# Kernel tuning notes

Measured on AMD Instinct MI355X. Metric: run time of the kernel, lower is better.

## Reference

```python
import jax, jax.numpy as jnp
import numpy as np

EMB = 1024
CTX = 32
F_IN, R, F_OUT = 1024, 16, 1024
N_EXP = 16
H1 = 2048   # expert / gating hidden
H2 = 512    # expert output width
B = 8


def _init(key, shape, fan_in):
    return jax.random.normal(key, shape, dtype=jnp.float32) / np.sqrt(fan_in)


def setup_inputs() -> dict:
    key = jax.random.key(0)
    ks = jax.random.split(key, 14)
    return {
        "s": jax.random.normal(ks[0], (B, EMB), dtype=jnp.float32),
        # gating: Linear(EMB,2048) -> ReLU -> Linear(2048,N_EXP) -> Softmax
        "Wg1": _init(ks[1], (EMB, H1), EMB),
        "bg1": jnp.zeros((H1,), jnp.float32),
        "Wg2": _init(ks[2], (H1, N_EXP), H1),
        "bg2": jnp.zeros((N_EXP,), jnp.float32),
        # experts (stacked): Linear(EMB+CTX,2048) -> ReLU -> Linear(2048,512)
        "W1": _init(ks[3], (N_EXP, EMB + CTX, H1), EMB + CTX),
        "b1": jnp.zeros((N_EXP, H1), jnp.float32),
        "W2": _init(ks[4], (N_EXP, H1, H2), H1),
        "b2": jnp.zeros((N_EXP, H2), jnp.float32),
        # decoders
        "WA": _init(ks[5], (H2, F_IN * R), H2),
        "bA": jnp.zeros((F_IN * R,), jnp.float32),
        "WB": _init(ks[6], (H2, R * F_OUT), H2),
        "bB": jnp.zeros((R * F_OUT,), jnp.float32),
    }


def reference(s, Wg1, bg1, Wg2, bg2, W1, b1, W2, b2, WA, bA, WB, bB):
    # gating weights over experts: [B, E]
    weights = jax.nn.softmax(jax.nn.relu(s @ Wg1 + bg1) @ Wg2 + bg2, axis=-1)

    # Expert layer-1. Input is concat([s, one_hot(c)]); since the context part
    # is a one-hot, its contribution is just a row of the context block of W1.
    W1s = W1[:, :EMB, :]              # [E, EMB, H1]
    W1c = W1[:, EMB:, :]              # [E, CTX, H1]
    base = jnp.einsum('bi,eih->ebh', s, W1s) + b1[:, None, :]   # [E, B, H1]
    # h[c,e,b,:] = relu(base[e,b,:] + W1c[e,c,:])
    h = jax.nn.relu(base[None] + jnp.transpose(W1c, (1, 0, 2))[:, :, None, :])  # [C,E,B,H1]

    # Expert layer-2: [C, E, B, H2]
    eo = jnp.einsum('cebh,ehd->cebd', h, W2) + b2[None, :, None, :]

    # softmax-weighted mixture over experts: [C, B, H2]
    z = jnp.einsum('be,cebd->cbd', weights, eo)

    A = (z @ WA + bA).reshape(CTX, B, F_IN, R)
    Bm = (z @ WB + bB).reshape(CTX, B, R, F_OUT)
    return A, Bm
```

## Files before the change

kernel.cpp:

```cpp
#include <hip/hip_runtime.h>
#include <hip/hip_bf16.h>

#define EMB 1024
#define CTX 32
#define NEXP 16
#define H1 2048
#define H2 512
#define NBIG 16384

typedef __attribute__((ext_vector_type(8))) short short8;
typedef __attribute__((ext_vector_type(4))) float floatx4;
typedef const __attribute__((address_space(1))) void* gas_t;
typedef __attribute__((address_space(3))) void* las_t;

__device__ __forceinline__ void gl16(const unsigned short* g, unsigned short* l) {
  __builtin_amdgcn_global_load_lds((gas_t)(const void*)g, (las_t)(void*)l, 16, 0, 0);
}

__device__ inline unsigned short bf_bits(float x) {
  unsigned u = __builtin_bit_cast(unsigned, x);
  u += 0x7fffu + ((u >> 16) & 1u);
  return (unsigned short)(u >> 16);
}
__device__ inline unsigned pk_bf16(float a, float b) {
  return (unsigned)bf_bits(a) | ((unsigned)bf_bits(b) << 16);
}

__global__ void __launch_bounds__(256) k_gate1(const float* __restrict__ s,
                                               const float* __restrict__ Wg1,
                                               const float* __restrict__ bg1,
                                               float* __restrict__ g1) {
  __shared__ float red[16][16][8];
  int t = threadIdx.x;
  int c = t & 15, kk = t >> 4;
  int h = blockIdx.x * 16 + c;
  float acc[8];
#pragma unroll
  for (int b = 0; b < 8; ++b) acc[b] = 0.f;
  int k0 = kk * 64;
  for (int k = k0; k < k0 + 64; ++k) {
    float w = Wg1[(size_t)k * H1 + h];
#pragma unroll
    for (int b = 0; b < 8; ++b) acc[b] += s[b * EMB + k] * w;
  }
#pragma unroll
  for (int b = 0; b < 8; ++b) red[kk][c][b] = acc[b];
  __syncthreads();
  if (t < 128) {
    int cc = t >> 3, b = t & 7;
    float v = 0.f;
#pragma unroll
    for (int q = 0; q < 16; ++q) v += red[q][cc][b];
    int hh = blockIdx.x * 16 + cc;
    v += bg1[hh];
    g1[b * H1 + hh] = fmaxf(v, 0.f);
  }
}

__global__ void __launch_bounds__(256) k_gate2(const float* __restrict__ g1,
                                               const float* __restrict__ Wg2,
                                               const float* __restrict__ bg2,
                                               float* __restrict__ logits) {
  __shared__ float red[256][8];
  int e = blockIdx.x, t = threadIdx.x;
  int k0 = t * 8;
  float wv[8];
#pragma unroll
  for (int j = 0; j < 8; ++j) wv[j] = Wg2[(size_t)(k0 + j) * NEXP + e];
  float acc[8];
#pragma unroll
  for (int b = 0; b < 8; ++b) {
    float4 ga = *(const float4*)&g1[b * H1 + k0];
    float4 gb = *(const float4*)&g1[b * H1 + k0 + 4];
    acc[b] = ga.x * wv[0] + ga.y * wv[1] + ga.z * wv[2] + ga.w * wv[3] +
             gb.x * wv[4] + gb.y * wv[5] + gb.z * wv[6] + gb.w * wv[7];
  }
#pragma unroll
  for (int b = 0; b < 8; ++b) red[t][b] = acc[b];
  __syncthreads();
  for (int off = 128; off > 0; off >>= 1) {
    if (t < off) {
#pragma unroll
      for (int b = 0; b < 8; ++b) red[t][b] += red[t + off][b];
    }
    __syncthreads();
  }
  if (t < 8) logits[t * NEXP + e] = red[0][t] + bg2[e];
}

__global__ void __launch_bounds__(512) k_base(const float* __restrict__ s,
                                              const float* __restrict__ W1,
                                              const float* __restrict__ b1,
                                              float* __restrict__ base) {
  __shared__ float sl[8 * EMB];
  __shared__ float red[8][64][17];
  int t = threadIdx.x;
  int ht = blockIdx.x;
  int e = blockIdx.y;
#pragma unroll
  for (int i = 0; i < 4; ++i) {
    int idx = (t + i * 512) * 4;
    *(float4*)&sl[idx] = *(const float4*)&s[idx];
  }
  __syncthreads();
  int hp = t & 63;
  int kk = t >> 6;
  int h = ht * 128 + hp * 2;
  const float* wp = W1 + (size_t)e * 1056 * H1 + h;
  float a0[8], a1[8];
#pragma unroll
  for (int b = 0; b < 8; ++b) { a0[b] = 0.f; a1[b] = 0.f; }
  int k0 = kk * 128;
  for (int k = k0; k < k0 + 128; ++k) {
    float2 w = *(const float2*)(wp + (size_t)k * H1);
#pragma unroll
    for (int b = 0; b < 8; ++b) {
      float sv = sl[b * EMB + k];
      a0[b] += sv * w.x;
      a1[b] += sv * w.y;
    }
  }
#pragma unroll
  for (int b = 0; b < 8; ++b) {
    red[kk][hp][b * 2] = a0[b];
    red[kk][hp][b * 2 + 1] = a1[b];
  }
  __syncthreads();
  if (t < 64) {
    int hh = ht * 128 + t * 2;
#pragma unroll
    for (int b = 0; b < 8; ++b) {
      float v0 = 0.f, v1 = 0.f;
#pragma unroll
      for (int q = 0; q < 8; ++q) {
        v0 += red[q][t][b * 2];
        v1 += red[q][t][b * 2 + 1];
      }
      float2 bv = *(const float2*)&b1[e * H1 + hh];
      float2 o;
      o.x = v0 + bv.x;
      o.y = v1 + bv.y;
      *(float2*)&base[(size_t)(e * 8 + b) * H1 + hh] = o;
    }
  }
}

__global__ void __launch_bounds__(256) k_packW(const float* __restrict__ src,
                                               unsigned short* __restrict__ dst,
                                               int Nsrc, int Ndst, int n_off,
                                               long sbs, long dbs) {
  __shared__ float tl[64][65];
  int nt = blockIdx.x, kb = blockIdx.y, bz = blockIdx.z, t = threadIdx.x;
  const float* S = src + (size_t)bz * sbs + (size_t)kb * 64 * Nsrc + nt * 64;
  int r = t >> 4, c4 = (t & 15) * 4;
#pragma unroll
  for (int i = 0; i < 4; ++i) {
    int row = r + i * 16;
    float4 v = *(const float4*)&S[(size_t)row * Nsrc + c4];
    *(float4*)&tl[row][c4] = v;
  }
  __syncthreads();
  int nl = t >> 2;
  int cb = (t & 3) * 2;
  int key = nl & 7;
  unsigned short* D = dst + (size_t)bz * dbs +
                      ((size_t)kb * Ndst + n_off + nt * 64 + nl) * 64;
#pragma unroll
  for (int j = 0; j < 2; ++j) {
    int cp = cb + j;
    int k0 = (cp ^ key) * 8;
    union { short8 v; unsigned u[4]; } p;
#pragma unroll
    for (int q = 0; q < 4; ++q)
      p.u[q] = pk_bf16(tl[k0 + 2 * q][nl], tl[k0 + 2 * q + 1][nl]);
    *(short8*)&D[cp * 8] = p.v;
  }
}

__global__ void __launch_bounds__(256) k_h(const float* __restrict__ base,
                                           const float* __restrict__ W1,
                                           unsigned short* __restrict__ h_t) {
  int c = blockIdx.x, e = blockIdx.y;
  int t = threadIdx.x;
  int b = t >> 5, l = t & 31;
  int m = c * 8 + b;
  const float* bp = base + ((size_t)e * 8 + b) * H1;
  const float* cp = W1 + ((size_t)e * 1056 + EMB + c) * H1;
  unsigned short* hp = h_t + (size_t)e * 32 * 256 * 64;
#pragma unroll
  for (int kc = 0; kc < 8; ++kc) {
    int k = kc * 256 + l * 8;
    int kb = k >> 6;
    int cc = (k >> 3) & 7;
    int cpx = cc ^ (b & 7);
    float4 x0 = *(const float4*)&bp[k];
    float4 x1 = *(const float4*)&bp[k + 4];
    float4 y0 = *(const float4*)&cp[k];
    float4 y1 = *(const float4*)&cp[k + 4];
    union { short8 v; unsigned u[4]; } p;
    p.u[0] = pk_bf16(fmaxf(x0.x + y0.x, 0.f), fmaxf(x0.y + y0.y, 0.f));
    p.u[1] = pk_bf16(fmaxf(x0.z + y0.z, 0.f), fmaxf(x0.w + y0.w, 0.f));
    p.u[2] = pk_bf16(fmaxf(x1.x + y1.x, 0.f), fmaxf(x1.y + y1.y, 0.f));
    p.u[3] = pk_bf16(fmaxf(x1.z + y1.z, 0.f), fmaxf(x1.w + y1.w, 0.f));
    *(short8*)&hp[((size_t)kb * 256 + m) * 64 + cpx * 8] = p.v;
  }
}

__global__ void __launch_bounds__(256) k_egemm(const unsigned short* __restrict__ h_t,
                                               const unsigned short* __restrict__ W2t,
                                               float* __restrict__ eo2) {
  __shared__ __align__(16) unsigned short As[4096];
  __shared__ __align__(16) unsigned short Bs[8192];
  int id = blockIdx.x;
  int e = (id & 7) + 8 * ((id >> 3) & 1);
  int r = id >> 4;
  int mt = r & 3, nt = (r >> 2) & 3, ks = (r >> 4) & 1;
  int t = threadIdx.x, lane = t & 63, w = t >> 6;
  int fr = lane & 15, quad = lane >> 4;
  int key = fr & 7;

  const unsigned short* hA = h_t + (size_t)e * 524288 + mt * 4096;
  const unsigned short* wB = W2t + (size_t)e * 1048576 + nt * 8192;

  floatx4 zero4 = {0.f, 0.f, 0.f, 0.f};
  floatx4 acc[4][2];
#pragma unroll
  for (int i = 0; i < 4; ++i) { acc[i][0] = zero4; acc[i][1] = zero4; }

  for (int i = 0; i < 16; ++i) {
    int kb = ks * 16 + i;
    __syncthreads();
    const unsigned short* asrc = hA + (size_t)kb * 16384 + t * 8;
    const unsigned short* bsrc = wB + (size_t)kb * 32768 + t * 8;
    gl16(asrc, &As[t * 8]);
    gl16(asrc + 2048, &As[t * 8 + 2048]);
    gl16(bsrc, &Bs[t * 8]);
    gl16(bsrc + 2048, &Bs[t * 8 + 2048]);
    gl16(bsrc + 4096, &Bs[t * 8 + 4096]);
    gl16(bsrc + 6144, &Bs[t * 8 + 6144]);
    __syncthreads();
#pragma unroll
    for (int ks2 = 0; ks2 < 2; ++ks2) {
      int cof = ((ks2 * 4 + quad) ^ key) * 8;
      short8 bf0 = *(const short8*)&Bs[w * 2048 + fr * 64 + cof];
      short8 bf1 = *(const short8*)&Bs[w * 2048 + 1024 + fr * 64 + cof];
#pragma unroll
      for (int rt = 0; rt < 4; ++rt) {
        short8 af = *(const short8*)&As[rt * 1024 + fr * 64 + cof];
        acc[rt][0] = __builtin_amdgcn_mfma_f32_16x16x32_bf16(af, bf0, acc[rt][0], 0, 0, 0);
        acc[rt][1] = __builtin_amdgcn_mfma_f32_16x16x32_bf16(af, bf1, acc[rt][1], 0, 0, 0);
      }
    }
  }
  float* op = eo2 + (size_t)ks * 2097152;
  int d0 = nt * 128 + w * 32 + fr;
#pragma unroll
  for (int nt2 = 0; nt2 < 2; ++nt2) {
    int d = d0 + nt2 * 16;
#pragma unroll
    for (int rt = 0; rt < 4; ++rt) {
#pragma unroll
      for (int i = 0; i < 4; ++i) {
        int gm = mt * 64 + rt * 16 + quad * 4 + i;
        op[(((size_t)(gm >> 3) * NEXP + e) * 8 + (gm & 7)) * H2 + d] = acc[rt][nt2][i];
      }
    }
  }
}

__global__ void __launch_bounds__(256) k_mix(const float* __restrict__ eo2,
                                             const float* __restrict__ logits,
                                             const float* __restrict__ b2,
                                             unsigned short* __restrict__ z_t) {
  int c = blockIdx.x, half = blockIdx.y, t = threadIdx.x;
  int b = t >> 5;
  int dc = half * 32 + (t & 31);
  int d0 = dc * 8;
  int m = c * 8 + b;
  float lg[16];
  float mx = -1e30f;
#pragma unroll
  for (int e = 0; e < 16; ++e) {
    lg[e] = logits[b * NEXP + e];
    mx = fmaxf(mx, lg[e]);
  }
  float sum = 0.f;
#pragma unroll
  for (int e = 0; e < 16; ++e) {
    lg[e] = __expf(lg[e] - mx);
    sum += lg[e];
  }
  float inv = 1.f / sum;
  float o[8];
#pragma unroll
  for (int j = 0; j < 8; ++j) o[j] = 0.f;
#pragma unroll
  for (int e = 0; e < 16; ++e) {
    float wl = lg[e] * inv;
    const float* p = &eo2[(((size_t)c * NEXP + e) * 8 + b) * H2 + d0];
    float4 x0 = *(const float4*)p;
    float4 x1 = *(const float4*)(p + 4);
    float4 y0 = *(const float4*)(p + 2097152);
    float4 y1 = *(const float4*)(p + 2097152 + 4);
    float4 v0 = *(const float4*)&b2[e * H2 + d0];
    float4 v1 = *(const float4*)&b2[e * H2 + d0 + 4];
    o[0] += wl * (x0.x + y0.x + v0.x);
    o[1] += wl * (x0.y + y0.y + v0.y);
    o[2] += wl * (x0.z + y0.z + v0.z);
    o[3] += wl * (x0.w + y0.w + v0.w);
    o[4] += wl * (x1.x + y1.x + v1.x);
    o[5] += wl * (x1.y + y1.y + v1.y);
    o[6] += wl * (x1.z + y1.z + v1.z);
    o[7] += wl * (x1.w + y1.w + v1.w);
  }
  union { short8 v; unsigned u[4]; } p;
#pragma unroll
  for (int q = 0; q < 4; ++q) p.u[q] = pk_bf16(o[2 * q], o[2 * q + 1]);
  int kb = dc >> 3;
  int cpx = (dc & 7) ^ (b & 7);
  *(short8*)&z_t[((size_t)kb * 256 + m) * 64 + cpx * 8] = p.v;
}

__global__ void __launch_bounds__(256) k_lora(const unsigned short* __restrict__ z_t,
                                              const unsigned short* __restrict__ Wab_t,
                                              const float* __restrict__ bA,
                                              const float* __restrict__ bB,
                                              float* __restrict__ out) {
  __shared__ __align__(16) unsigned short As[8192];
  __shared__ __align__(16) unsigned short Bs[8192];
  int id = blockIdx.x;
  int nt = id & 255, mt = id >> 8;
  int t = threadIdx.x, lane = t & 63, w = t >> 6;
  int fr = lane & 15, quad = lane >> 4;
  int key = fr & 7;

  const unsigned short* zA = z_t + mt * 8192;
  const unsigned short* wB = Wab_t + (size_t)nt * 8192;

  floatx4 zero4 = {0.f, 0.f, 0.f, 0.f};
  floatx4 acc[8][2];
#pragma unroll
  for (int i = 0; i < 8; ++i) { acc[i][0] = zero4; acc[i][1] = zero4; }

  for (int kb = 0; kb < 8; ++kb) {
    __syncthreads();
    const unsigned short* asrc = zA + (size_t)kb * 16384 + t * 8;
    const unsigned short* bsrc = wB + (size_t)kb * 2097152 + t * 8;
    gl16(asrc, &As[t * 8]);
    gl16(asrc + 2048, &As[t * 8 + 2048]);
    gl16(asrc + 4096, &As[t * 8 + 4096]);
    gl16(asrc + 6144, &As[t * 8 + 6144]);
    gl16(bsrc, &Bs[t * 8]);
    gl16(bsrc + 2048, &Bs[t * 8 + 2048]);
    gl16(bsrc + 4096, &Bs[t * 8 + 4096]);
    gl16(bsrc + 6144, &Bs[t * 8 + 6144]);
    __syncthreads();
#pragma unroll
    for (int ks2 = 0; ks2 < 2; ++ks2) {
      int cof = ((ks2 * 4 + quad) ^ key) * 8;
      short8 bf0 = *(const short8*)&Bs[w * 2048 + fr * 64 + cof];
      short8 bf1 = *(const short8*)&Bs[w * 2048 + 1024 + fr * 64 + cof];
#pragma unroll
      for (int rt = 0; rt < 8; ++rt) {
        short8 af = *(const short8*)&As[rt * 1024 + fr * 64 + cof];
        acc[rt][0] = __builtin_amdgcn_mfma_f32_16x16x32_bf16(af, bf0, acc[rt][0], 0, 0, 0);
        acc[rt][1] = __builtin_amdgcn_mfma_f32_16x16x32_bf16(af, bf1, acc[rt][1], 0, 0, 0);
      }
    }
  }
  int nb0 = nt * 128 + w * 32 + fr;
#pragma unroll
  for (int nt2 = 0; nt2 < 2; ++nt2) {
    int n = nb0 + nt2 * 16;
    int ms = n >> 14;
    int nn = n & (NBIG - 1);
    float bv = ms ? bB[nn] : bA[nn];
    float* o = out + (size_t)ms * 4194304 + nn;
#pragma unroll
    for (int rt = 0; rt < 8; ++rt) {
#pragma unroll
      for (int i = 0; i < 4; ++i) {
        int m = mt * 128 + rt * 16 + quad * 4 + i;
        o[(size_t)m * NBIG] = acc[rt][nt2][i] + bv;
      }
    }
  }
}

extern "C" void kernel_launch(void* const* d_in, const int* in_sizes, int n_in,
                              void* d_out, int out_size, void* d_ws, size_t ws_size,
                              hipStream_t stream) {
  const float* s = (const float*)d_in[0];
  const float* Wg1 = (const float*)d_in[1];
  const float* bg1 = (const float*)d_in[2];
  const float* Wg2 = (const float*)d_in[3];
  const float* bg2 = (const float*)d_in[4];
  const float* W1 = (const float*)d_in[5];
  const float* b1 = (const float*)d_in[6];
  const float* W2 = (const float*)d_in[7];
  const float* b2 = (const float*)d_in[8];
  const float* WA = (const float*)d_in[9];
  const float* bA = (const float*)d_in[10];
  const float* WB = (const float*)d_in[11];
  const float* bB = (const float*)d_in[12];
  float* out = (float*)d_out;

  char* ws = (char*)d_ws;
  float* g1 = (float*)(ws);
  float* logits = (float*)(ws + 65536);
  float* base = (float*)(ws + 131072);
  unsigned short* h_t = (unsigned short*)(ws + 1179648);
  float* eo2 = (float*)(ws + 17956864);
  unsigned short* z_t = (unsigned short*)(ws + 34734080);
  unsigned short* W2t = (unsigned short*)(ws + 34996224);
  unsigned short* Wab_t = (unsigned short*)(ws + 68550656);

  k_gate1<<<128, 256, 0, stream>>>(s, Wg1, bg1, g1);
  k_gate2<<<16, 256, 0, stream>>>(g1, Wg2, bg2, logits);
  k_base<<<dim3(16, 16), 512, 0, stream>>>(s, W1, b1, base);
  k_h<<<dim3(32, 16), 256, 0, stream>>>(base, W1, h_t);
  k_packW<<<dim3(8, 32, 16), 256, 0, stream>>>(W2, W2t, H2, H2, 0,
                                               (long)H1 * H2, (long)H1 * H2);
  k_packW<<<dim3(256, 8, 1), 256, 0, stream>>>(WA, Wab_t, NBIG, 2 * NBIG, 0, 0, 0);
  k_packW<<<dim3(256, 8, 1), 256, 0, stream>>>(WB, Wab_t, NBIG, 2 * NBIG, NBIG, 0, 0);
  k_egemm<<<512, 256, 0, stream>>>(h_t, W2t, eo2);
  k_mix<<<dim3(32, 2), 256, 0, stream>>>(eo2, logits, b2, z_t);
  k_lora<<<512, 256, 0, stream>>>(z_t, Wab_t, bA, bB, out);
}
```

Baseline: 396.2 us.

## Fuse hidden-activation build into expert GEMM and WA/WB packing into LoRA GEMM

The separate k_h kernel that materialized the bf16 hidden activations is removed. The expert GEMM now computes relu(base + W1 context row) on the fly into shared memory. The two k_packW launches for WA/WB are also removed: the LoRA GEMM reads the fp32 decoder weights directly, converts them to bf16 and stores them swizzled in LDS. Each LoRA block now covers all 256 rows, so each weight column is read once. Both GEMMs move to 512-thread blocks with new tile shapes. This removes large intermediate round trips through memory, but the LoRA B loads are strided row reads by column, which may coalesce less well.

New measurement: 390.0 us. About the same (-1.6%).

```diff
diff --git a/kernel.cpp b/kernel.cpp
--- a/kernel.cpp
+++ b/kernel.cpp
@@ -177,92 +177,77 @@
   }
 }
 
-__global__ void __launch_bounds__(256) k_h(const float* __restrict__ base,
-                                           const float* __restrict__ W1,
-                                           unsigned short* __restrict__ h_t) {
-  int c = blockIdx.x, e = blockIdx.y;
-  int t = threadIdx.x;
-  int b = t >> 5, l = t & 31;
-  int m = c * 8 + b;
-  const float* bp = base + ((size_t)e * 8 + b) * H1;
-  const float* cp = W1 + ((size_t)e * 1056 + EMB + c) * H1;
-  unsigned short* hp = h_t + (size_t)e * 32 * 256 * 64;
-#pragma unroll
-  for (int kc = 0; kc < 8; ++kc) {
-    int k = kc * 256 + l * 8;
-    int kb = k >> 6;
-    int cc = (k >> 3) & 7;
-    int cpx = cc ^ (b & 7);
-    float4 x0 = *(const float4*)&bp[k];
-    float4 x1 = *(const float4*)&bp[k + 4];
-    float4 y0 = *(const float4*)&cp[k];
-    float4 y1 = *(const float4*)&cp[k + 4];
-    union { short8 v; unsigned u[4]; } p;
-    p.u[0] = pk_bf16(fmaxf(x0.x + y0.x, 0.f), fmaxf(x0.y + y0.y, 0.f));
-    p.u[1] = pk_bf16(fmaxf(x0.z + y0.z, 0.f), fmaxf(x0.w + y0.w, 0.f));
-    p.u[2] = pk_bf16(fmaxf(x1.x + y1.x, 0.f), fmaxf(x1.y + y1.y, 0.f));
-    p.u[3] = pk_bf16(fmaxf(x1.z + y1.z, 0.f), fmaxf(x1.w + y1.w, 0.f));
-    *(short8*)&hp[((size_t)kb * 256 + m) * 64 + cpx * 8] = p.v;
-  }
-}
-
-__global__ void __launch_bounds__(256) k_egemm(const unsigned short* __restrict__ h_t,
-                                               const unsigned short* __restrict__ W2t,
-                                               float* __restrict__ eo2) {
+__global__ void __launch_bounds__(512) k_egemm2(const float* __restrict__ base,
+                                                const float* __restrict__ W1,
+                                                const unsigned short* __restrict__ W2t,
+                                                float* __restrict__ eo2) {
   __shared__ __align__(16) unsigned short As[4096];
-  __shared__ __align__(16) unsigned short Bs[8192];
+  __shared__ __align__(16) unsigned short Bs[16384];
   int id = blockIdx.x;
-  int e = (id & 7) + 8 * ((id >> 3) & 1);
-  int r = id >> 4;
-  int mt = r & 3, nt = (r >> 2) & 3, ks = (r >> 4) & 1;
+  int mt = id >> 6, rem = id & 63;
+  int e = rem >> 2, nt = (rem >> 1) & 1, ks = rem & 1;
   int t = threadIdx.x, lane = t & 63, w = t >> 6;
-  int fr = lane & 15, quad = lane >> 4;
-  int key = fr & 7;
-
-  const unsigned short* hA = h_t + (size_t)e * 524288 + mt * 4096;
-  const unsigned short* wB = W2t + (size_t)e * 1048576 + nt * 8192;
+  int wm = w >> 2, wn = w & 3;
+  int fr = lane & 15, quad = lane >> 4, key = fr & 7;
+
+  int am = t >> 3;
+  int ak = (t & 7) * 8;
+  const float* bp = base + ((size_t)e * 8 + (am & 7)) * H1;
+  const float* cp = W1 + ((size_t)e * 1056 + EMB + mt * 8 + (am >> 3)) * H1;
+  unsigned short* adst = &As[am * 64 + (((t & 7) ^ (am & 7)) * 8)];
+  const unsigned short* wBe = W2t + (size_t)e * 1048576 + (size_t)nt * 16384;
 
   floatx4 zero4 = {0.f, 0.f, 0.f, 0.f};
-  floatx4 acc[4][2];
-#pragma unroll
-  for (int i = 0; i < 4; ++i) { acc[i][0] = zero4; acc[i][1] = zero4; }
+  floatx4 acc[2][4];
+#pragma unroll
+  for (int i = 0; i < 2; ++i)
+#pragma unroll
+    for (int j = 0; j < 4; ++j) acc[i][j] = zero4;
 
   for (int i = 0; i < 16; ++i) {
     int kb = ks * 16 + i;
     __syncthreads();
-    const unsigned short* asrc = hA + (size_t)kb * 16384 + t * 8;
-    const unsigned short* bsrc = wB + (size_t)kb * 32768 + t * 8;
-    gl16(asrc, &As[t * 8]);
-    gl16(asrc + 2048, &As[t * 8 + 2048]);
+    const unsigned short* bsrc = wBe + (size_t)kb * 32768 + t * 8;
     gl16(bsrc, &Bs[t * 8]);
-    gl16(bsrc + 2048, &Bs[t * 8 + 2048]);
     gl16(bsrc + 4096, &Bs[t * 8 + 4096]);
-    gl16(bsrc + 6144, &Bs[t * 8 + 6144]);
+    gl16(bsrc + 8192, &Bs[t * 8 + 8192]);
+    gl16(bsrc + 12288, &Bs[t * 8 + 12288]);
+    int k0 = kb * 64 + ak;
+    float4 x0 = *(const float4*)&bp[k0];
+    float4 x1 = *(const float4*)&bp[k0 + 4];
+    float4 y0 = *(const float4*)&cp[k0];
+    float4 y1 = *(const float4*)&cp[k0 + 4];
+    union { short8 v; unsigned u[4]; } pq;
+    pq.u[0] = pk_bf16(fmaxf(x0.x + y0.x, 0.f), fmaxf(x0.y + y0.y, 0.f));
+    pq.u[1] = pk_bf16(fmaxf(x0.z + y0.z, 0.f), fmaxf(x0.w + y0.w, 0.f));
+    pq.u[2] = pk_bf16(fmaxf(x1.x + y1.x, 0.f), fmaxf(x1.y + y1.y, 0.f));
+    pq.u[3] = pk_bf16(fmaxf(x1.z + y1.z, 0.f), fmaxf(x1.w + y1.w, 0.f));
+    *(short8*)adst = pq.v;
     __syncthreads();
 #pragma unroll
     for (int ks2 = 0; ks2 < 2; ++ks2) {
       int cof = ((ks2 * 4 + quad) ^ key) * 8;
-      short8 bf0 = *(const short8*)&Bs[w * 2048 + fr * 64 + cof];
-      short8 bf1 = *(const short8*)&Bs[w * 2048 + 1024 + fr * 64 + cof];
-#pragma unroll
-      for (int rt = 0; rt < 4; ++rt) {
-        short8 af = *(const short8*)&As[rt * 1024 + fr * 64 + cof];
-        acc[rt][0] = __builtin_amdgcn_mfma_f32_16x16x32_bf16(af, bf0, acc[rt][0], 0, 0, 0);
-        acc[rt][1] = __builtin_amdgcn_mfma_f32_16x16x32_bf16(af, bf1, acc[rt][1], 0, 0, 0);
+      short8 a0 = *(const short8*)&As[(wm * 32 + fr) * 64 + cof];
+      short8 a1 = *(const short8*)&As[(wm * 32 + 16 + fr) * 64 + cof];
+#pragma unroll
+      for (int nj = 0; nj < 4; ++nj) {
+        short8 bf = *(const short8*)&Bs[(wn * 64 + nj * 16 + fr) * 64 + cof];
+        acc[0][nj] = __builtin_amdgcn_mfma_f32_16x16x32_bf16(a0, bf, acc[0][nj], 0, 0, 0);
+        acc[1][nj] = __builtin_amdgcn_mfma_f32_16x16x32_bf16(a1, bf, acc[1][nj], 0, 0, 0);
       }
     }
   }
   float* op = eo2 + (size_t)ks * 2097152;
-  int d0 = nt * 128 + w * 32 + fr;
-#pragma unroll
-  for (int nt2 = 0; nt2 < 2; ++nt2) {
-    int d = d0 + nt2 * 16;
-#pragma unroll
-    for (int rt = 0; rt < 4; ++rt) {
-#pragma unroll
-      for (int i = 0; i < 4; ++i) {
-        int gm = mt * 64 + rt * 16 + quad * 4 + i;
-        op[(((size_t)(gm >> 3) * NEXP + e) * 8 + (gm & 7)) * H2 + d] = acc[rt][nt2][i];
+  int d0 = nt * 256 + wn * 64 + fr;
+#pragma unroll
+  for (int nj = 0; nj < 4; ++nj) {
+    int d = d0 + nj * 16;
+#pragma unroll
+    for (int rt = 0; rt < 2; ++rt) {
+#pragma unroll
+      for (int i2 = 0; i2 < 4; ++i2) {
+        int gm = mt * 64 + wm * 32 + rt * 16 + quad * 4 + i2;
+        op[(((size_t)(gm >> 3) * NEXP + e) * 8 + (gm & 7)) * H2 + d] = acc[rt][nj][i2];
       }
     }
   }
@@ -321,67 +306,82 @@
   *(short8*)&z_t[((size_t)kb * 256 + m) * 64 + cpx * 8] = p.v;
 }
 
-__global__ void __launch_bounds__(256) k_lora(const unsigned short* __restrict__ z_t,
-                                              const unsigned short* __restrict__ Wab_t,
-                                              const float* __restrict__ bA,
-                                              const float* __restrict__ bB,
-                                              float* __restrict__ out) {
-  __shared__ __align__(16) unsigned short As[8192];
+__global__ void __launch_bounds__(512) k_lora2(const unsigned short* __restrict__ z_t,
+                                               const float* __restrict__ WA,
+                                               const float* __restrict__ WB,
+                                               const float* __restrict__ bA,
+                                               const float* __restrict__ bB,
+                                               float* __restrict__ out) {
+  __shared__ __align__(16) unsigned short As[16384];
   __shared__ __align__(16) unsigned short Bs[8192];
-  int id = blockIdx.x;
-  int nt = id & 255, mt = id >> 8;
+  int nt = blockIdx.x;
   int t = threadIdx.x, lane = t & 63, w = t >> 6;
-  int fr = lane & 15, quad = lane >> 4;
-  int key = fr & 7;
-
-  const unsigned short* zA = z_t + mt * 8192;
-  const unsigned short* wB = Wab_t + (size_t)nt * 8192;
+  int wm = w >> 1, wn = w & 1;
+  int fr = lane & 15, quad = lane >> 4, key = fr & 7;
+  int ms = nt >> 7;
+  const float* Wsrc = ms ? WB : WA;
+  int col0 = (nt & 127) * 128;
+  int bn = t & 127, kg = t >> 7;
+  const float* bw = Wsrc + col0 + bn;
+  unsigned short* bd0 = &Bs[bn * 64 + (((kg * 2) ^ (bn & 7)) * 8)];
+  unsigned short* bd1 = &Bs[bn * 64 + (((kg * 2 + 1) ^ (bn & 7)) * 8)];
 
   floatx4 zero4 = {0.f, 0.f, 0.f, 0.f};
-  floatx4 acc[8][2];
-#pragma unroll
-  for (int i = 0; i < 8; ++i) { acc[i][0] = zero4; acc[i][1] = zero4; }
+  floatx4 acc[4][4];
+#pragma unroll
+  for (int i = 0; i < 4; ++i)
+#pragma unroll
+    for (int j = 0; j < 4; ++j) acc[i][j] = zero4;
 
   for (int kb = 0; kb < 8; ++kb) {
     __syncthreads();
-    const unsigned short* asrc = zA + (size_t)kb * 16384 + t * 8;
-    const unsigned short* bsrc = wB + (size_t)kb * 2097152 + t * 8;
+    const unsigned short* asrc = z_t + (size_t)kb * 16384 + t * 8;
     gl16(asrc, &As[t * 8]);
-    gl16(asrc + 2048, &As[t * 8 + 2048]);
     gl16(asrc + 4096, &As[t * 8 + 4096]);
-    gl16(asrc + 6144, &As[t * 8 + 6144]);
-    gl16(bsrc, &Bs[t * 8]);
-    gl16(bsrc + 2048, &Bs[t * 8 + 2048]);
-    gl16(bsrc + 4096, &Bs[t * 8 + 4096]);
-    gl16(bsrc + 6144, &Bs[t * 8 + 6144]);
+    gl16(asrc + 8192, &As[t * 8 + 8192]);
+    gl16(asrc + 12288, &As[t * 8 + 12288]);
+    const float* bk = bw + (size_t)(kb * 64 + kg * 16) * NBIG;
+    float v[16];
+#pragma unroll
+    for (int kr = 0; kr < 16; ++kr) v[kr] = bk[(size_t)kr * NBIG];
+    union { short8 s; unsigned u[4]; } q0, q1;
+#pragma unroll
+    for (int q = 0; q < 4; ++q) {
+      q0.u[q] = pk_bf16(v[2 * q], v[2 * q + 1]);
+      q1.u[q] = pk_bf16(v[8 + 2 * q], v[9 + 2 * q]);
+    }
+    *(short8*)bd0 = q0.s;
+    *(short8*)bd1 = q1.s;
     __syncthreads();
 #pragma unroll
     for (int ks2 = 0; ks2 < 2; ++ks2) {
       int cof = ((ks2 * 4 + quad) ^ key) * 8;
-      short8 bf0 = *(const short8*)&Bs[w * 2048 + fr * 64 + cof];
-      short8 bf1 = *(const short8*)&Bs[w * 2048 + 1024 + fr * 64 + cof];
-#pragma unroll
-      for (int rt = 0; rt < 8; ++rt) {
-        short8 af = *(const short8*)&As[rt * 1024 + fr * 64 + cof];
+      short8 bf0 = *(const short8*)&Bs[(wn * 64 + fr) * 64 + cof];
+      short8 bf1 = *(const short8*)&Bs[(wn * 64 + 16 + fr) * 64 + cof];
+      short8 bf2 = *(const short8*)&Bs[(wn * 64 + 32 + fr) * 64 + cof];
+      short8 bf3 = *(const short8*)&Bs[(wn * 64 + 48 + fr) * 64 + cof];
+#pragma unroll
+      for (int rt = 0; rt < 4; ++rt) {
+        short8 af = *(const short8*)&As[(wm * 64 + rt * 16 + fr) * 64 + cof];
         acc[rt][0] = __builtin_amdgcn_mfma_f32_16x16x32_bf16(af, bf0, acc[rt][0], 0, 0, 0);
         acc[rt][1] = __builtin_amdgcn_mfma_f32_16x16x32_bf16(af, bf1, acc[rt][1], 0, 0, 0);
+        acc[rt][2] = __builtin_amdgcn_mfma_f32_16x16x32_bf16(af, bf2, acc[rt][2], 0, 0, 0);
+        acc[rt][3] = __builtin_amdgcn_mfma_f32_16x16x32_bf16(af, bf3, acc[rt][3], 0, 0, 0);
       }
     }
   }
-  int nb0 = nt * 128 + w * 32 + fr;
-#pragma unroll
-  for (int nt2 = 0; nt2 < 2; ++nt2) {
-    int n = nb0 + nt2 * 16;
-    int ms = n >> 14;
-    int nn = n & (NBIG - 1);
-    float bv = ms ? bB[nn] : bA[nn];
-    float* o = out + (size_t)ms * 4194304 + nn;
-#pragma unroll
-    for (int rt = 0; rt < 8; ++rt) {
-#pragma unroll
-      for (int i = 0; i < 4; ++i) {
-        int m = mt * 128 + rt * 16 + quad * 4 + i;
-        o[(size_t)m * NBIG] = acc[rt][nt2][i] + bv;
+  const float* bias = ms ? bB : bA;
+  float* obase = out + (size_t)ms * 4194304;
+#pragma unroll
+  for (int nj = 0; nj < 4; ++nj) {
+    int nn = col0 + wn * 64 + nj * 16 + fr;
+    float bv = bias[nn];
+#pragma unroll
+    for (int rt = 0; rt < 4; ++rt) {
+#pragma unroll
+      for (int i2 = 0; i2 < 4; ++i2) {
+        int m = wm * 64 + rt * 16 + quad * 4 + i2;
+        obase[(size_t)m * NBIG + nn] = acc[rt][nj][i2] + bv;
       }
     }
   }
@@ -409,21 +409,16 @@
   float* g1 = (float*)(ws);
   float* logits = (float*)(ws + 65536);
   float* base = (float*)(ws + 131072);
-  unsigned short* h_t = (unsigned short*)(ws + 1179648);
-  float* eo2 = (float*)(ws + 17956864);
-  unsigned short* z_t = (unsigned short*)(ws + 34734080);
-  unsigned short* W2t = (unsigned short*)(ws + 34996224);
-  unsigned short* Wab_t = (unsigned short*)(ws + 68550656);
+  float* eo2 = (float*)(ws + 1179648);
+  unsigned short* z_t = (unsigned short*)(ws + 17956864);
+  unsigned short* W2t = (unsigned short*)(ws + 18219008);
 
   k_gate1<<<128, 256, 0, stream>>>(s, Wg1, bg1, g1);
   k_gate2<<<16, 256, 0, stream>>>(g1, Wg2, bg2, logits);
   k_base<<<dim3(16, 16), 512, 0, stream>>>(s, W1, b1, base);
-  k_h<<<dim3(32, 16), 256, 0, stream>>>(base, W1, h_t);
   k_packW<<<dim3(8, 32, 16), 256, 0, stream>>>(W2, W2t, H2, H2, 0,
                                                (long)H1 * H2, (long)H1 * H2);
-  k_packW<<<dim3(256, 8, 1), 256, 0, stream>>>(WA, Wab_t, NBIG, 2 * NBIG, 0, 0, 0);
-  k_packW<<<dim3(256, 8, 1), 256, 0, stream>>>(WB, Wab_t, NBIG, 2 * NBIG, NBIG, 0, 0);
-  k_egemm<<<512, 256, 0, stream>>>(h_t, W2t, eo2);
+  k_egemm2<<<256, 512, 0, stream>>>(base, W1, W2t, eo2);
   k_mix<<<dim3(32, 2), 256, 0, stream>>>(eo2, logits, b2, z_t);
-  k_lora<<<512, 256, 0, stream>>>(z_t, Wab_t, bA, bB, out);
-}
+  k_lora2<<<256, 512, 0, stream>>>(z_t, WA, WB, bA, bB, out);
+}
```
